# Kernel tuning notes

Measured on AMD Instinct MI355X. Metric: run time of the kernel, lower is better.

The kernel has to match this reference:

```python
import jax, jax.numpy as jnp
import numpy as np

KERNEL_SIZE = 7      # odd, per assert in __init__
MAX_VAL = 1e4        # kornia morphology default max_val


def setup_inputs() -> dict:
    key = jax.random.key(0)
    kx, ka, kb, kc = jax.random.split(key, 4)
    x = jax.random.normal(kx, (8, 64, 256, 256), dtype=jnp.float32)
    k1 = jax.random.uniform(ka, (1,), dtype=jnp.float32)
    k2 = jax.random.uniform(kb, (1,), dtype=jnp.float32)
    k3 = jax.random.uniform(kc, (1,), dtype=jnp.float32)
    return {"x": x, "k1": k1, "k2": k2, "k3": k3}


def _structuring_element(k1, k2, k3):
    k = KERNEL_SIZE
    # torch.arange(-k//2 + 1, k//2 + 1) with floor-div == -(k//2)..k//2 for odd k
    c = jnp.arange(-(k // 2), k // 2 + 1, dtype=jnp.float32)
    xg, yg = jnp.meshgrid(c, c, indexing='xy')
    se = k1[0] * xg ** 2 + 2.0 * k2[0] * xg * yg + k3[0] * yg ** 2
    se = se / se.max()
    return -se  # (k, k)


def reference(x, k1, k2, k3):
    k = KERNEL_SIZE
    se = _structuring_element(k1, k2, k3)
    # flat kernel of ones with center zeroed -> center tap masked to -max_val
    mask = np.ones((k, k), dtype=bool)
    mask[k // 2, k // 2] = False
    neighborhood = jnp.where(jnp.asarray(mask), se, -MAX_VAL)
    nb = neighborhood[::-1, ::-1]  # kornia dilation flips the neighborhood

    pad = k // 2
    # geodesic border for dilation: pad with -max_val
    xp = jnp.pad(x, ((0, 0), (0, 0), (pad, pad), (pad, pad)),
                 constant_values=-MAX_VAL)
    H, W = x.shape[-2], x.shape[-1]
    # fused running max over the k*k taps; avoids materializing the unfold
    out = jnp.full_like(x, -jnp.inf)
    for i in range(k):
        for j in range(k):
            out = jnp.maximum(out, xp[..., i:i + H, j:j + W] + nb[i, j])
    return out
```

## Files before the change

kernel.cpp:

```cpp
#include <hip/hip_runtime.h>


#define MAXV 10000.0f

constexpr int H = 256;
constexpr int W = 256;

typedef float vf4 __attribute__((ext_vector_type(4)));
typedef float vf2 __attribute__((ext_vector_type(2)));

__global__ __launch_bounds__(256, 8) void morpho_kernel(
    const float* __restrict__ x,
    const float* __restrict__ k1p,
    const float* __restrict__ k2p,
    const float* __restrict__ k3p,
    float* __restrict__ out) {
  const int tid = threadIdx.x;
  const int lane = tid & 63;
  const int wid = __builtin_amdgcn_readfirstlane(tid >> 6);
  const int p = blockIdx.x >> 2;
  const int ty0 = (blockIdx.x & 3) * 64;

  const float* __restrict__ xp = x + (size_t)p * (H * W);
  float* __restrict__ op = out + (size_t)p * (H * W);

  const float k1v = k1p[0], k2v = k2p[0], k3v = k3p[0];
  const int ia = lane >> 3, ib = lane & 7;
  const float xg = (float)(((ib < 6) ? ib : 6) - 3);
  const float yg = (float)(((ia < 6) ? ia : 6) - 3);
  const float sev = k1v * (xg * xg) + 2.0f * k2v * (xg * yg) + k3v * (yg * yg);
  float mx = sev;
#pragma unroll
  for (int off = 32; off; off >>= 1) mx = fmaxf(mx, __shfl_xor(mx, off, 64));
  const float wv = 0.0f - sev * (1.0f / mx);

  vf2 wp[7][3];
  float w6[7];
#pragma unroll
  for (int d = 0; d < 7; ++d) {
#pragma unroll
    for (int m = 0; m < 3; ++m) {
      vf2 pr;
      pr.x = __int_as_float(__builtin_amdgcn_readlane(__float_as_int(wv), d * 8 + 2 * m));
      pr.y = __int_as_float(__builtin_amdgcn_readlane(__float_as_int(wv), d * 8 + 2 * m + 1));
      wp[d][m] = pr;
    }
    w6[d] = __int_as_float(__builtin_amdgcn_readlane(__float_as_int(wv), d * 8 + 6));
  }
  wp[3][1].y = -MAXV;

  const bool l0 = (lane == 0);
  const bool l63 = (lane == 63);
  const int o1 = lane * 4;
  const int o0 = l0 ? o1 : o1 - 4;
  const int o2 = l63 ? o1 : o1 + 4;

  for (int k = 0; k < 4; ++k) {
    const int y0c = ty0 + 4 * wid + 16 * k;

    float acc[4][4];
#pragma unroll
    for (int t = 0; t < 4; ++t)
#pragma unroll
      for (int c = 0; c < 4; ++c) acc[t][c] = -INFINITY;

#pragma unroll
    for (int iy = 0; iy < 10; ++iy) {
      const int r = y0c - 3 + iy;
      if (r < 0 || r >= H) continue;
      const float* __restrict__ rb = xp + r * W;

      vf4 q0 = *reinterpret_cast<const vf4*>(rb + o0);
      vf4 q1 = *reinterpret_cast<const vf4*>(rb + o1);
      vf4 q2 = *reinterpret_cast<const vf4*>(rb + o2);

      q0.y = l0 ? -MAXV : q0.y;
      q0.z = l0 ? -MAXV : q0.z;
      q0.w = l0 ? -MAXV : q0.w;
      q2.x = l63 ? -MAXV : q2.x;
      q2.y = l63 ? -MAXV : q2.y;
      q2.z = l63 ? -MAXV : q2.z;

      const vf2 O0 = __builtin_shufflevector(q0, q0, 1, 2);
      const vf2 O1 = __builtin_shufflevector(q0, q1, 3, 4);
      const vf2 O2 = __builtin_shufflevector(q1, q1, 1, 2);
      const vf2 O3 = __builtin_shufflevector(q1, q2, 3, 4);
      const vf2 E0 = __builtin_shufflevector(q0, q0, 2, 3);
      const vf2 E1 = __builtin_shufflevector(q1, q1, 0, 1);
      const vf2 E2 = __builtin_shufflevector(q1, q1, 2, 3);
      const vf2 E3 = __builtin_shufflevector(q2, q2, 0, 1);

      const vf2 P[4][3] = {{O0, O1, O2}, {E0, E1, E2}, {O1, O2, O3}, {E1, E2, E3}};
      const float T[4] = {q1.w, q2.x, q2.y, q2.z};

#pragma unroll
      for (int t = 0; t < 4; ++t) {
        const int dyr = iy - t;
        if (dyr < 0 || dyr > 6) continue;
#pragma unroll
        for (int c = 0; c < 4; ++c) {
          const vf2 a = P[c][0] + wp[dyr][0];
          const vf2 b = P[c][1] + wp[dyr][1];
          const vf2 g = P[c][2] + wp[dyr][2];
          const float s6 = T[c] + w6[dyr];
          const float m0 = fmaxf(fmaxf(a.x, a.y), b.x);
          const float m1 = fmaxf(fmaxf(b.y, g.x), g.y);
          const float m2 = fmaxf(fmaxf(s6, m0), m1);
          acc[t][c] = fmaxf(acc[t][c], m2);
        }
      }
    }

#pragma unroll
    for (int t = 0; t < 4; ++t) {
      vf4 v;
      v.x = acc[t][0];
      v.y = acc[t][1];
      v.z = acc[t][2];
      v.w = acc[t][3];
      __builtin_nontemporal_store(
          v, reinterpret_cast<vf4*>(&op[(y0c + t) * W + lane * 4]));
    }
  }
}

extern "C" void kernel_launch(void* const* d_in, const int* in_sizes, int n_in,
                              void* d_out, int out_size, void* d_ws, size_t ws_size,
                              hipStream_t stream) {
  const float* x = (const float*)d_in[0];
  const float* k1 = (const float*)d_in[1];
  const float* k2 = (const float*)d_in[2];
  const float* k3 = (const float*)d_in[3];
  float* outp = (float*)d_out;

  const int planes = 8 * 64;
  const int blocks = planes * 4;
  morpho_kernel<<<dim3(blocks), dim3(256), 0, stream>>>(x, k1, k2, k3, outp);
}
```

Before: 254.3 us.

## Stream 16 contiguous rows per wave with rolling accumulators and prefetch ring

Each wave now handles 16 consecutive output rows and sweeps its input rows once, instead of four separate 4-row chunks that each reloaded a 10-row halo. A 3-slot register ring prefetches input rows two iterations ahead, and a 7-slot rotating accumulator array writes each output row as soon as it is complete. This cuts redundant global loads from 40 per wave to 22 and overlaps loads with compute. The cost is more registers, so the occupancy hint drops from 8 to 4 waves, which may hide less latency.

```diff
diff --git a/kernel.cpp b/kernel.cpp
--- a/kernel.cpp
+++ b/kernel.cpp
@@ -9,7 +9,7 @@
 typedef float vf4 __attribute__((ext_vector_type(4)));
 typedef float vf2 __attribute__((ext_vector_type(2)));
 
-__global__ __launch_bounds__(256, 8) void morpho_kernel(
+__global__ __launch_bounds__(256, 4) void morpho_kernel(
     const float* __restrict__ x,
     const float* __restrict__ k1p,
     const float* __restrict__ k2p,
@@ -19,7 +19,7 @@
   const int lane = tid & 63;
   const int wid = __builtin_amdgcn_readfirstlane(tid >> 6);
   const int p = blockIdx.x >> 2;
-  const int ty0 = (blockIdx.x & 3) * 64;
+  const int y0w = (blockIdx.x & 3) * 64 + wid * 16;
 
   const float* __restrict__ xp = x + (size_t)p * (H * W);
   float* __restrict__ op = out + (size_t)p * (H * W);
@@ -55,24 +55,46 @@
   const int o0 = l0 ? o1 : o1 - 4;
   const int o2 = l63 ? o1 : o1 + 4;
 
-  for (int k = 0; k < 4; ++k) {
-    const int y0c = ty0 + 4 * wid + 16 * k;
+  vf4 ring[3][3];
+  {
+    const int r0 = (y0w - 3 < 0) ? 0 : y0w - 3;
+    const float* __restrict__ rb = xp + r0 * W;
+    ring[0][0] = *reinterpret_cast<const vf4*>(rb + o0);
+    ring[0][1] = *reinterpret_cast<const vf4*>(rb + o1);
+    ring[0][2] = *reinterpret_cast<const vf4*>(rb + o2);
+  }
+  {
+    const int r1 = (y0w - 2 < 0) ? 0 : y0w - 2;
+    const float* __restrict__ rb = xp + r1 * W;
+    ring[1][0] = *reinterpret_cast<const vf4*>(rb + o0);
+    ring[1][1] = *reinterpret_cast<const vf4*>(rb + o1);
+    ring[1][2] = *reinterpret_cast<const vf4*>(rb + o2);
+  }
 
-    float acc[4][4];
+  float acc[7][4];
 #pragma unroll
-    for (int t = 0; t < 4; ++t)
+  for (int s = 0; s < 7; ++s)
 #pragma unroll
-      for (int c = 0; c < 4; ++c) acc[t][c] = -INFINITY;
+    for (int c = 0; c < 4; ++c) acc[s][c] = -INFINITY;
 
 #pragma unroll
-    for (int iy = 0; iy < 10; ++iy) {
-      const int r = y0c - 3 + iy;
-      if (r < 0 || r >= H) continue;
-      const float* __restrict__ rb = xp + r * W;
+  for (int iy = 0; iy < 22; ++iy) {
+    if (iy < 20) {
+      int rp = y0w - 1 + iy;
+      rp = (rp < 0) ? 0 : ((rp > H - 1) ? H - 1 : rp);
+      const float* __restrict__ rb = xp + rp * W;
+      const int sl = (iy + 2) % 3;
+      ring[sl][0] = *reinterpret_cast<const vf4*>(rb + o0);
+      ring[sl][1] = *reinterpret_cast<const vf4*>(rb + o1);
+      ring[sl][2] = *reinterpret_cast<const vf4*>(rb + o2);
+    }
 
-      vf4 q0 = *reinterpret_cast<const vf4*>(rb + o0);
-      vf4 q1 = *reinterpret_cast<const vf4*>(rb + o1);
-      vf4 q2 = *reinterpret_cast<const vf4*>(rb + o2);
+    const int r = y0w - 3 + iy;
+    if ((iy >= 3 && iy <= 18) || (r >= 0 && r < H)) {
+      const int cs = iy % 3;
+      vf4 q0 = ring[cs][0];
+      vf4 q1 = ring[cs][1];
+      vf4 q2 = ring[cs][2];
 
       q0.y = l0 ? -MAXV : q0.y;
       q0.z = l0 ? -MAXV : q0.z;
@@ -94,32 +116,38 @@
       const float T[4] = {q1.w, q2.x, q2.y, q2.z};
 
 #pragma unroll
-      for (int t = 0; t < 4; ++t) {
-        const int dyr = iy - t;
-        if (dyr < 0 || dyr > 6) continue;
+      for (int dd = 0; dd < 7; ++dd) {
+        const int t = iy - dd;
+        if (t < 0 || t > 15) continue;
+        const int st = t % 7;
 #pragma unroll
         for (int c = 0; c < 4; ++c) {
-          const vf2 a = P[c][0] + wp[dyr][0];
-          const vf2 b = P[c][1] + wp[dyr][1];
-          const vf2 g = P[c][2] + wp[dyr][2];
-          const float s6 = T[c] + w6[dyr];
+          const vf2 a = P[c][0] + wp[dd][0];
+          const vf2 b = P[c][1] + wp[dd][1];
+          const vf2 g = P[c][2] + wp[dd][2];
+          const float s6 = T[c] + w6[dd];
           const float m0 = fmaxf(fmaxf(a.x, a.y), b.x);
           const float m1 = fmaxf(fmaxf(b.y, g.x), g.y);
           const float m2 = fmaxf(fmaxf(s6, m0), m1);
-          acc[t][c] = fmaxf(acc[t][c], m2);
+          acc[st][c] = fmaxf(acc[st][c], m2);
         }
       }
     }
 
+    if (iy >= 6) {
+      const int tr = iy - 6;
+      const int st = tr % 7;
+      vf4 v;
+      v.x = acc[st][0];
+      v.y = acc[st][1];
+      v.z = acc[st][2];
+      v.w = acc[st][3];
+      __builtin_nontemporal_store(
+          v, reinterpret_cast<vf4*>(&op[(y0w + tr) * W + o1]));
+      if (iy <= 14) {
 #pragma unroll
-    for (int t = 0; t < 4; ++t) {
-      vf4 v;
-      v.x = acc[t][0];
-      v.y = acc[t][1];
-      v.z = acc[t][2];
-      v.w = acc[t][3];
-      __builtin_nontemporal_store(
-          v, reinterpret_cast<vf4*>(&op[(y0c + t) * W + lane * 4]));
+        for (int c = 0; c < 4; ++c) acc[st][c] = -INFINITY;
+      }
     }
   }
 }
```

Result: no change. 249.4 us (-1.9%).
